# Kernel optimization log

Hardware: AMD Instinct MI355X
Metric: run time of the kernel (lower is better)

## Reference

```python
import jax, jax.numpy as jnp
import numpy as np

CPV = 64  # cpv_size; output_size = CPV*(CPV+1)//2 = 2080

def _tri_indices(cpv):
    # Reproduce the torch nested-loop scatter order:
    # for idx_x in range(cpv): for idx_y in range(cpv-idx_x): col = cpv-1-idx_y
    rows = np.repeat(np.arange(cpv), cpv - np.arange(cpv))
    cols = np.concatenate([np.arange(cpv - 1, i - 1, -1) for i in range(cpv)])
    return jnp.asarray(rows), jnp.asarray(cols)


def setup_inputs() -> dict:
    key = jax.random.key(0)
    ks = jax.random.split(key, 12)
    B, D_in, H, L = 8192, 1024, 2048, CPV * (CPV + 1) // 2
    s = lambda fan_in: 1.0 / np.sqrt(fan_in)
    return {
        "x":   jax.random.normal(ks[0], (B, D_in), jnp.float32),
        "W1":  jax.random.uniform(ks[1], (D_in, H), jnp.float32, -s(D_in), s(D_in)),
        "b1":  jnp.zeros((H,), jnp.float32),
        "W2":  jax.random.uniform(ks[2], (H, H), jnp.float32, -s(H), s(H)),
        "b2":  jnp.zeros((H,), jnp.float32),
        "W21": jax.random.uniform(ks[3], (H, H), jnp.float32, -s(H), s(H)),
        "b21": jnp.zeros((H,), jnp.float32),
        "W22": jax.random.uniform(ks[4], (H, H), jnp.float32, -s(H), s(H)),
        "b22": jnp.zeros((H,), jnp.float32),
        "W3":  jax.random.uniform(ks[5], (H, L), jnp.float32, -s(H), s(H)),
        "b3":  jnp.zeros((L,), jnp.float32),
    }


def reference(x, W1, b1, W2, b2, W21, b21, W22, b22, W3, b3):
    lrelu = lambda t: jax.nn.leaky_relu(t, 0.01)
    h = lrelu(x @ W1 + b1)
    h = lrelu(h @ W2 + b2)
    h = lrelu(h @ W21 + b21)
    h = lrelu(h @ W22 + b22)
    y = h @ W3 + b3  # [B, L] with L = CPV*(CPV+1)//2
    rows, cols = _tri_indices(CPV)
    is_diag = rows == cols  # diagonal entries are abs'ed (negated when <= 0)
    vals = jnp.where(is_diag[None, :] & (y <= 0), -y, y)
    B = y.shape[0]
    M = jnp.zeros((B, CPV, CPV), y.dtype).at[:, rows, cols].set(vals)
    return jnp.transpose(M, (1, 2, 0))  # torch stacks per-example matrices on dim=2
```

## Files before the change

### kernel.cpp

```cpp
#include <hip/hip_runtime.h>
#include <hip/hip_bf16.h>
#include <stdint.h>

typedef short short8 __attribute__((ext_vector_type(8)));
typedef float f32x4  __attribute__((ext_vector_type(4)));

typedef __attribute__((address_space(1))) uint32_t u32_g;
typedef __attribute__((address_space(3))) uint32_t u32_l;

#define BM 256
#define BN 256
#define BK 32
#define SLOTB 32768
#define BOFF  16384

__device__ __forceinline__ void gld_lds16(const void* g, const void* l) {
  __builtin_amdgcn_global_load_lds((u32_g*)(uintptr_t)g, (u32_l*)(uintptr_t)l, 16, 0, 0);
}

template <int FINAL>
__global__ __launch_bounds__(512, 2) void gemm_k(
    const __hip_bfloat16* __restrict__ A,
    const __hip_bfloat16* __restrict__ BT,
    const float* __restrict__ bias,
    __hip_bfloat16* __restrict__ Cb,
    float* __restrict__ Cf,
    const int* __restrict__ tbl,
    int K, int Nreal)
{
  __shared__ __attribute__((aligned(16))) char smem[3 * SLOTB];

  const int tid  = threadIdx.x;
  const int lane = tid & 63;
  const int l15  = lane & 15;
  const int quad = lane >> 4;
  const int wave = tid >> 6;
  const int wm   = (wave >> 2) * 128;
  const int wn   = (wave & 3) * 64;

  const int bm = blockIdx.x * BM;
  const int bn = blockIdx.y * BN;

  const int arow = wm + l15;
  const uint32_t aoff = (uint32_t)arow * 64u + (uint32_t)(((quad + (arow >> 1)) & 3) << 4);
  const int brow = wn + l15;
  const uint32_t boff = BOFF + (uint32_t)brow * 64u + (uint32_t)(((quad + (brow >> 1)) & 3) << 4);

  const __hip_bfloat16* ag[2];
  const __hip_bfloat16* bg[2];
  uint32_t dA[2], dB[2];
#pragma unroll
  for (int c = 0; c < 2; ++c) {
    int ci  = tid + 512 * c;
    int row = ci >> 2;
    int gc  = ((ci & 3) - (row >> 1)) & 3;
    ag[c] = A  + (size_t)(bm + row) * K + gc * 8;
    bg[c] = BT + (size_t)(bn + row) * K + gc * 8;
    dA[c] = (uint32_t)ci * 16u;
    dB[c] = BOFF + (uint32_t)ci * 16u;
  }

  f32x4 acc[8][4];
#pragma unroll
  for (int i = 0; i < 8; ++i)
#pragma unroll
    for (int j = 0; j < 4; ++j)
      acc[i][j] = (f32x4){0.f, 0.f, 0.f, 0.f};

  const int nk = K >> 5;

#pragma unroll
  for (int t = 0; t < 2; ++t) {
    char* stb = smem + t * SLOTB;
#pragma unroll
    for (int c = 0; c < 2; ++c) {
      gld_lds16(ag[c], stb + dA[c]);
      gld_lds16(bg[c], stb + dB[c]);
      ag[c] += BK;
      bg[c] += BK;
    }
  }

  int cur = 0, nst = 2;
  for (int kt = 0; kt < nk; ++kt) {
    if (kt < nk - 1) asm volatile("s_waitcnt vmcnt(4) lgkmcnt(0)" ::: "memory");
    else             asm volatile("s_waitcnt vmcnt(0) lgkmcnt(0)" ::: "memory");
    __builtin_amdgcn_s_barrier();
    asm volatile("" ::: "memory");

    const char* rb  = smem + cur * SLOTB;
    char*       stb = smem + nst * SLOTB;

    if (kt < nk - 2) {
#pragma unroll
      for (int c = 0; c < 2; ++c) {
        gld_lds16(ag[c], stb + dA[c]);
        gld_lds16(bg[c], stb + dB[c]);
        ag[c] += BK;
        bg[c] += BK;
      }
    }

    short8 bf[4], af[4];
#pragma unroll
    for (int j = 0; j < 4; ++j) bf[j] = *(const short8*)(rb + boff + j * 1024);
#pragma unroll
    for (int i = 0; i < 4; ++i) af[i] = *(const short8*)(rb + aoff + i * 1024);
    __builtin_amdgcn_s_setprio(1);
#pragma unroll
    for (int i = 0; i < 4; ++i)
#pragma unroll
      for (int j = 0; j < 4; ++j)
        acc[i][j] = __builtin_amdgcn_mfma_f32_16x16x32_bf16(af[i], bf[j], acc[i][j], 0, 0, 0);
    __builtin_amdgcn_s_setprio(0);

    short8 af2[4];
#pragma unroll
    for (int i = 0; i < 4; ++i) af2[i] = *(const short8*)(rb + aoff + 4096 + i * 1024);
    __builtin_amdgcn_s_setprio(1);
#pragma unroll
    for (int i = 0; i < 4; ++i)
#pragma unroll
      for (int j = 0; j < 4; ++j)
        acc[i + 4][j] = __builtin_amdgcn_mfma_f32_16x16x32_bf16(af2[i], bf[j], acc[i + 4][j], 0, 0, 0);
    __builtin_amdgcn_s_setprio(0);

    cur = (cur == 2) ? 0 : cur + 1;
    nst = (nst == 2) ? 0 : nst + 1;
  }

  if (FINAL == 0) {
#pragma unroll
    for (int j = 0; j < 4; ++j) {
      int   n  = bn + wn + j * 16 + l15;
      float bv = bias[n];
#pragma unroll
      for (int i = 0; i < 8; ++i) {
        int m0 = bm + wm + i * 16 + quad * 4;
#pragma unroll
        for (int r = 0; r < 4; ++r) {
          float v = acc[i][j][r] + bv;
          v = (v > 0.f) ? v : 0.01f * v;
          Cb[(size_t)(m0 + r) * 2048 + n] = __float2bfloat16(v);
        }
      }
    }
  } else {
#pragma unroll
    for (int j = 0; j < 4; ++j) {
      int n = bn + wn + j * 16 + l15;
      if (n < Nreal) {
        float bv   = bias[n];
        int  code  = tbl[n];
        int  dst   = code & 4095;
        bool diag  = (code & 4096) != 0;
        int  mir   = ((dst & 63) << 6) | (dst >> 6);
        const f32x4 z = (f32x4){0.f, 0.f, 0.f, 0.f};
#pragma unroll
        for (int i = 0; i < 8; ++i) {
          int m0 = bm + wm + i * 16 + quad * 4;
          f32x4 pk;
#pragma unroll
          for (int r = 0; r < 4; ++r) {
            float v = acc[i][j][r] + bv;
            if (diag) v = fabsf(v);
            pk[r] = v;
          }
          *reinterpret_cast<f32x4*>(Cf + (size_t)dst * 8192 + m0) = pk;
          if (!diag)
            *reinterpret_cast<f32x4*>(Cf + (size_t)mir * 8192 + m0) = z;
        }
      }
    }
  }
}

__global__ void transpose_k(const float* __restrict__ in,
                            __hip_bfloat16* __restrict__ out,
                            int K, int N)
{
  __shared__ __hip_bfloat16 t[32][33];
  const int n0 = blockIdx.x * 32;
  const int k0 = blockIdx.y * 32;
  const int tx = threadIdx.x, ty = threadIdx.y;
  const __hip_bfloat16 zero = __float2bfloat16(0.f);
#pragma unroll
  for (int r = 0; r < 32; r += 8) {
    int k = k0 + ty + r, n = n0 + tx;
    t[ty + r][tx] = (n < N) ? __float2bfloat16(in[(size_t)k * N + n]) : zero;
  }
  __syncthreads();
#pragma unroll
  for (int r = 0; r < 32; r += 8) {
    int n = n0 + ty + r;
    out[(size_t)n * K + k0 + tx] = t[tx][ty + r];
  }
}

__global__ void cvt_k(const float* __restrict__ in,
                      __hip_bfloat16* __restrict__ out, int n)
{
  int i = (blockIdx.x * 256 + threadIdx.x) * 4;
  if (i >= n) return;
  float4 v = *reinterpret_cast<const float4*>(in + i);
  union { unsigned short us[4]; uint2 v2; } pk;
  __hip_bfloat16 h;
  h = __float2bfloat16(v.x); pk.us[0] = *reinterpret_cast<unsigned short*>(&h);
  h = __float2bfloat16(v.y); pk.us[1] = *reinterpret_cast<unsigned short*>(&h);
  h = __float2bfloat16(v.z); pk.us[2] = *reinterpret_cast<unsigned short*>(&h);
  h = __float2bfloat16(v.w); pk.us[3] = *reinterpret_cast<unsigned short*>(&h);
  *reinterpret_cast<uint2*>(out + i) = pk.v2;
}

__global__ void table_k(int* __restrict__ tbl)
{
  int l = blockIdx.x * 64 + threadIdx.x;
  if (l >= 2080) return;
  int r = 0, s = 0;
  while (s + (64 - r) <= l) { s += 64 - r; ++r; }
  int c = 63 - (l - s);
  tbl[l] = (r * 64 + c) | ((r == c) ? 4096 : 0);
}

extern "C" void kernel_launch(void* const* d_in, const int* in_sizes, int n_in,
                              void* d_out, int out_size, void* d_ws, size_t ws_size,
                              hipStream_t stream)
{
  const float* x   = (const float*)d_in[0];
  const float* W1  = (const float*)d_in[1];
  const float* b1  = (const float*)d_in[2];
  const float* W2  = (const float*)d_in[3];
  const float* b2  = (const float*)d_in[4];
  const float* W21 = (const float*)d_in[5];
  const float* b21 = (const float*)d_in[6];
  const float* W22 = (const float*)d_in[7];
  const float* b22 = (const float*)d_in[8];
  const float* W3  = (const float*)d_in[9];
  const float* b3  = (const float*)d_in[10];
  float* out = (float*)d_out;

  char* ws = (char*)d_ws;
  __hip_bfloat16* act0 = (__hip_bfloat16*)(ws);
  __hip_bfloat16* act1 = (__hip_bfloat16*)(ws + ((size_t)32 << 20));
  __hip_bfloat16* xb   = act1;
  __hip_bfloat16* W1T  = (__hip_bfloat16*)(ws + ((size_t)64 << 20));
  __hip_bfloat16* W2T  = (__hip_bfloat16*)(ws + ((size_t)68 << 20));
  __hip_bfloat16* W21T = (__hip_bfloat16*)(ws + ((size_t)76 << 20));
  __hip_bfloat16* W22T = (__hip_bfloat16*)(ws + ((size_t)84 << 20));
  __hip_bfloat16* W3T  = (__hip_bfloat16*)(ws + ((size_t)92 << 20));
  int*            tbl  = (int*)(ws + ((size_t)101 << 20));

  table_k<<<33, 64, 0, stream>>>(tbl);

  cvt_k<<<8192, 256, 0, stream>>>(x, xb, 8192 * 1024);

  dim3 tb(32, 8);
  transpose_k<<<dim3(64, 32), tb, 0, stream>>>(W1,  W1T,  1024, 2048);
  transpose_k<<<dim3(64, 64), tb, 0, stream>>>(W2,  W2T,  2048, 2048);
  transpose_k<<<dim3(64, 64), tb, 0, stream>>>(W21, W21T, 2048, 2048);
  transpose_k<<<dim3(64, 64), tb, 0, stream>>>(W22, W22T, 2048, 2048);
  transpose_k<<<dim3(72, 64), tb, 0, stream>>>(W3,  W3T,  2048, 2080);

  gemm_k<0><<<dim3(32, 8), 512, 0, stream>>>(xb,   W1T,  b1,  act0, nullptr, nullptr, 1024, 2048);
  gemm_k<0><<<dim3(32, 8), 512, 0, stream>>>(act0, W2T,  b2,  act1, nullptr, nullptr, 2048, 2048);
  gemm_k<0><<<dim3(32, 8), 512, 0, stream>>>(act1, W21T, b21, act0, nullptr, nullptr, 2048, 2048);
  gemm_k<0><<<dim3(32, 8), 512, 0, stream>>>(act0, W22T, b22, act1, nullptr, nullptr, 2048, 2048);
  gemm_k<1><<<dim3(32, 9), 512, 0, stream>>>(act1, W3T,  b3,  nullptr, out,  tbl,     2048, 2080);
}
```

Measured before the change: 607.3 us.

## Restructure GEMM main loop into 4-phase ping-pong with BK=64 double buffering

Replaces the BK=32 triple-buffered loop with a BK=64 double-buffered scheme over 128KB of LDS. Each K-step is split into four MFMA phases interleaved with LDS reads and staged global-to-LDS loads of the next tiles in half-tile chunks. Barriers separate the phases. The goal is to overlap memory traffic with compute and to halve the loop-iteration overhead. It adds more barriers per iteration and uses the full LDS, which may limit occupancy to one block per CU despite launch_bounds(512,2).

```diff
diff --git a/kernel.cpp b/kernel.cpp
--- a/kernel.cpp
+++ b/kernel.cpp
@@ -10,9 +10,6 @@
 
 #define BM 256
 #define BN 256
-#define BK 32
-#define SLOTB 32768
-#define BOFF  16384
 
 __device__ __forceinline__ void gld_lds16(const void* g, const void* l) {
   __builtin_amdgcn_global_load_lds((u32_g*)(uintptr_t)g, (u32_l*)(uintptr_t)l, 16, 0, 0);
@@ -28,7 +25,7 @@
     const int* __restrict__ tbl,
     int K, int Nreal)
 {
-  __shared__ __attribute__((aligned(16))) char smem[3 * SLOTB];
+  __shared__ __attribute__((aligned(16))) char smem[131072];
 
   const int tid  = threadIdx.x;
   const int lane = tid & 63;
@@ -41,24 +38,34 @@
   const int bm = blockIdx.x * BM;
   const int bn = blockIdx.y * BN;
 
-  const int arow = wm + l15;
-  const uint32_t aoff = (uint32_t)arow * 64u + (uint32_t)(((quad + (arow >> 1)) & 3) << 4);
-  const int brow = wn + l15;
-  const uint32_t boff = BOFF + (uint32_t)brow * 64u + (uint32_t)(((quad + (brow >> 1)) & 3) << 4);
-
-  const __hip_bfloat16* ag[2];
-  const __hip_bfloat16* bg[2];
-  uint32_t dA[2], dB[2];
-#pragma unroll
-  for (int c = 0; c < 2; ++c) {
-    int ci  = tid + 512 * c;
-    int row = ci >> 2;
-    int gc  = ((ci & 3) - (row >> 1)) & 3;
-    ag[c] = A  + (size_t)(bm + row) * K + gc * 8;
-    bg[c] = BT + (size_t)(bn + row) * K + gc * 8;
-    dA[c] = (uint32_t)ci * 16u;
-    dB[c] = BOFF + (uint32_t)ci * 16u;
-  }
+  const uint32_t aB  = (uint32_t)(wm >> 7) * 16384u + (uint32_t)l15 * 128u;
+  const uint32_t bB  = 32768u + (uint32_t)(wn >> 7) * 16384u
+                     + (uint32_t)((wn & 127) + l15) * 128u;
+  const uint32_t cs0 = (uint32_t)((quad + l15) & 7) * 16u;
+  const uint32_t cs1 = (uint32_t)((quad + l15 + 4) & 7) * 16u;
+
+  const int r0  = tid >> 3,          r1  = (tid + 512) >> 3;
+  const int gc0 = ((tid & 7) - r0) & 7, gc1 = (((tid + 512) & 7) - r1) & 7;
+  const __hip_bfloat16* aP0 = A  + (size_t)(bm + r0) * K + gc0 * 8;
+  const __hip_bfloat16* aP1 = A  + (size_t)(bm + r1) * K + gc1 * 8;
+  const __hip_bfloat16* bP0 = BT + (size_t)(bn + r0) * K + gc0 * 8;
+  const __hip_bfloat16* bP1 = BT + (size_t)(bn + r1) * K + gc1 * 8;
+  const uint32_t dst0 = (uint32_t)tid * 16u;
+  const uint32_t dst1 = dst0 + 8192u;
+  const size_t   hK   = (size_t)128 * K;
+
+  auto stgA = [&](int q, int h) {
+    char*  d  = smem + (q & 1) * 65536 + h * 16384;
+    size_t ko = (size_t)q * 64 + (size_t)h * hK;
+    gld_lds16(aP0 + ko, d + dst0);
+    gld_lds16(aP1 + ko, d + dst1);
+  };
+  auto stgB = [&](int q, int h) {
+    char*  d  = smem + (q & 1) * 65536 + 32768 + h * 16384;
+    size_t ko = (size_t)q * 64 + (size_t)h * hK;
+    gld_lds16(bP0 + ko, d + dst0);
+    gld_lds16(bP1 + ko, d + dst1);
+  };
 
   f32x4 acc[8][4];
 #pragma unroll
@@ -67,66 +74,97 @@
     for (int j = 0; j < 4; ++j)
       acc[i][j] = (f32x4){0.f, 0.f, 0.f, 0.f};
 
-  const int nk = K >> 5;
-
-#pragma unroll
-  for (int t = 0; t < 2; ++t) {
-    char* stb = smem + t * SLOTB;
-#pragma unroll
-    for (int c = 0; c < 2; ++c) {
-      gld_lds16(ag[c], stb + dA[c]);
-      gld_lds16(bg[c], stb + dB[c]);
-      ag[c] += BK;
-      bg[c] += BK;
-    }
-  }
-
-  int cur = 0, nst = 2;
-  for (int kt = 0; kt < nk; ++kt) {
-    if (kt < nk - 1) asm volatile("s_waitcnt vmcnt(4) lgkmcnt(0)" ::: "memory");
-    else             asm volatile("s_waitcnt vmcnt(0) lgkmcnt(0)" ::: "memory");
-    __builtin_amdgcn_s_barrier();
-    asm volatile("" ::: "memory");
-
-    const char* rb  = smem + cur * SLOTB;
-    char*       stb = smem + nst * SLOTB;
-
-    if (kt < nk - 2) {
-#pragma unroll
-      for (int c = 0; c < 2; ++c) {
-        gld_lds16(ag[c], stb + dA[c]);
-        gld_lds16(bg[c], stb + dB[c]);
-        ag[c] += BK;
-        bg[c] += BK;
-      }
-    }
-
-    short8 bf[4], af[4];
-#pragma unroll
-    for (int j = 0; j < 4; ++j) bf[j] = *(const short8*)(rb + boff + j * 1024);
-#pragma unroll
-    for (int i = 0; i < 4; ++i) af[i] = *(const short8*)(rb + aoff + i * 1024);
+  const int NQ = K >> 6;
+
+  stgB(0, 0); stgB(0, 1); stgA(0, 0); stgA(0, 1); stgB(1, 0); stgB(1, 1);
+  asm volatile("s_waitcnt vmcnt(4)" ::: "memory");
+  __builtin_amdgcn_s_barrier();
+
+  for (int q = 0; q < NQ; ++q) {
+    const char* rb = smem + (q & 1) * 65536;
+    short8 a0[2][4], a1[2][4], bl[2][2], br[2][2];
+
+#pragma unroll
+    for (int s = 0; s < 2; ++s) {
+      const uint32_t cs = s ? cs1 : cs0;
+#pragma unroll
+      for (int i = 0; i < 4; ++i) a0[s][i] = *(const short8*)(rb + aB + i * 2048 + cs);
+#pragma unroll
+      for (int j = 0; j < 2; ++j) bl[s][j] = *(const short8*)(rb + bB + j * 2048 + cs);
+    }
+    if (q + 1 < NQ) stgA(q + 1, 0);
+    asm volatile("s_waitcnt lgkmcnt(8)" ::: "memory");
+    __builtin_amdgcn_s_barrier();
+    asm volatile("s_waitcnt lgkmcnt(0)" ::: "memory");
+    __builtin_amdgcn_sched_barrier(0);
     __builtin_amdgcn_s_setprio(1);
 #pragma unroll
-    for (int i = 0; i < 4; ++i)
-#pragma unroll
-      for (int j = 0; j < 4; ++j)
-        acc[i][j] = __builtin_amdgcn_mfma_f32_16x16x32_bf16(af[i], bf[j], acc[i][j], 0, 0, 0);
+    for (int s = 0; s < 2; ++s)
+#pragma unroll
+      for (int i = 0; i < 4; ++i)
+#pragma unroll
+        for (int j = 0; j < 2; ++j)
+          acc[i][j] = __builtin_amdgcn_mfma_f32_16x16x32_bf16(a0[s][i], bl[s][j], acc[i][j], 0, 0, 0);
     __builtin_amdgcn_s_setprio(0);
-
-    short8 af2[4];
-#pragma unroll
-    for (int i = 0; i < 4; ++i) af2[i] = *(const short8*)(rb + aoff + 4096 + i * 1024);
+    __builtin_amdgcn_s_barrier();
+
+#pragma unroll
+    for (int s = 0; s < 2; ++s) {
+      const uint32_t cs = s ? cs1 : cs0;
+#pragma unroll
+      for (int j = 0; j < 2; ++j) br[s][j] = *(const short8*)(rb + bB + (j + 2) * 2048 + cs);
+    }
+    if (q + 1 < NQ) stgA(q + 1, 1);
+    __builtin_amdgcn_s_barrier();
+    asm volatile("s_waitcnt lgkmcnt(0)" ::: "memory");
+    __builtin_amdgcn_sched_barrier(0);
     __builtin_amdgcn_s_setprio(1);
 #pragma unroll
-    for (int i = 0; i < 4; ++i)
-#pragma unroll
-      for (int j = 0; j < 4; ++j)
-        acc[i + 4][j] = __builtin_amdgcn_mfma_f32_16x16x32_bf16(af2[i], bf[j], acc[i + 4][j], 0, 0, 0);
+    for (int s = 0; s < 2; ++s)
+#pragma unroll
+      for (int i = 0; i < 4; ++i)
+#pragma unroll
+        for (int j = 0; j < 2; ++j)
+          acc[i][j + 2] = __builtin_amdgcn_mfma_f32_16x16x32_bf16(a0[s][i], br[s][j], acc[i][j + 2], 0, 0, 0);
     __builtin_amdgcn_s_setprio(0);
-
-    cur = (cur == 2) ? 0 : cur + 1;
-    nst = (nst == 2) ? 0 : nst + 1;
+    __builtin_amdgcn_s_barrier();
+
+#pragma unroll
+    for (int s = 0; s < 2; ++s) {
+      const uint32_t cs = s ? cs1 : cs0;
+#pragma unroll
+      for (int i = 0; i < 4; ++i) a1[s][i] = *(const short8*)(rb + aB + (i + 4) * 2048 + cs);
+    }
+    if (q + 2 < NQ) stgB(q + 2, 0);
+    __builtin_amdgcn_s_barrier();
+    asm volatile("s_waitcnt lgkmcnt(0)" ::: "memory");
+    __builtin_amdgcn_sched_barrier(0);
+    __builtin_amdgcn_s_setprio(1);
+#pragma unroll
+    for (int s = 0; s < 2; ++s)
+#pragma unroll
+      for (int i = 0; i < 4; ++i)
+#pragma unroll
+        for (int j = 0; j < 2; ++j)
+          acc[i + 4][j + 2] = __builtin_amdgcn_mfma_f32_16x16x32_bf16(a1[s][i], br[s][j], acc[i + 4][j + 2], 0, 0, 0);
+    __builtin_amdgcn_s_setprio(0);
+    __builtin_amdgcn_s_barrier();
+
+    if (q + 2 < NQ) stgB(q + 2, 1);
+    if (q < NQ - 2)       asm volatile("s_waitcnt vmcnt(4)" ::: "memory");
+    else if (q == NQ - 2) asm volatile("s_waitcnt vmcnt(0)" ::: "memory");
+    __builtin_amdgcn_s_barrier();
+    __builtin_amdgcn_sched_barrier(0);
+    __builtin_amdgcn_s_setprio(1);
+#pragma unroll
+    for (int s = 0; s < 2; ++s)
+#pragma unroll
+      for (int i = 0; i < 4; ++i)
+#pragma unroll
+        for (int j = 0; j < 2; ++j)
+          acc[i + 4][j] = __builtin_amdgcn_mfma_f32_16x16x32_bf16(a1[s][i], bl[s][j], acc[i + 4][j], 0, 0, 0);
+    __builtin_amdgcn_s_setprio(0);
+    __builtin_amdgcn_s_barrier();
   }
 
   if (FINAL == 0) {
```

Result: no change. 613.8 us (+1.1%).
